# Kernel tuning notes

Hardware: AMD Instinct MI355X
Metric: run time of the kernel (lower is better)

## Reference

```python
import jax, jax.numpy as jnp
import numpy as np

N, E, D, H, O = 100000, 1600000, 128, 128, 64


def setup_inputs() -> dict:
    key = jax.random.key(0)
    ks = jax.random.split(key, 9)
    x = jax.random.normal(ks[0], (N, D), dtype=jnp.float32)
    edge_index = jax.random.randint(ks[1], (2, E), 0, N, dtype=jnp.int64)
    edge_weight = jax.random.normal(ks[2], (E,), dtype=jnp.float32)
    s1 = 1.0 / np.sqrt(D)
    s2 = 1.0 / np.sqrt(H)
    W_rel1 = jax.random.normal(ks[3], (D, H), dtype=jnp.float32) * s1
    b_rel1 = jnp.zeros((H,), dtype=jnp.float32)
    W_root1 = jax.random.normal(ks[4], (D, H), dtype=jnp.float32) * s1
    W_rel2 = jax.random.normal(ks[5], (H, O), dtype=jnp.float32) * s2
    b_rel2 = jnp.zeros((O,), dtype=jnp.float32)
    W_root2 = jax.random.normal(ks[6], (H, O), dtype=jnp.float32) * s2
    return {"x": x, "edge_weight": edge_weight, "edge_index": edge_index,
            "W_rel1": W_rel1, "b_rel1": b_rel1, "W_root1": W_root1,
            "W_rel2": W_rel2, "b_rel2": b_rel2, "W_root2": W_root2}


def _graph_conv(h, src, dst, ew, W_rel, b_rel, W_root):
    # message: gather source features, scale by edge weight  [E, d]
    msg = h[src] * ew[:, None]
    # aggregate: sum messages into destination nodes  [N, d]
    aggr = jax.ops.segment_sum(msg, dst, num_segments=N)
    # GraphConv: lin_rel(aggr) + lin_root(h)
    return aggr @ W_rel + b_rel + h @ W_root


def reference(x, edge_weight, edge_index, W_rel1, b_rel1, W_root1, W_rel2, b_rel2, W_root2):
    src, dst = edge_index[0], edge_index[1]
    ew = jax.nn.sigmoid(edge_weight)  # edge_weighted=True path, applied once
    h = jax.nn.relu(_graph_conv(x, src, dst, ew, W_rel1, b_rel1, W_root1))
    out = _graph_conv(h, src, dst, ew, W_rel2, b_rel2, W_root2)
    return out
```

## Files before the change

### kernel.cpp

```cpp
#include <hip/hip_runtime.h>

#define NN 100000
#define EE 1600000
#define DD 128
#define HH 128
#define OO 64

#define NPART 8
#define CAP 32
#define MAX_OVF 16384
#define CSTRIDE 16

typedef unsigned short u16;
typedef __attribute__((ext_vector_type(8))) short bf16x8;
typedef __attribute__((ext_vector_type(4))) float f32x4;

__device__ __forceinline__ u16 f2b(float f) {
  union { float f; unsigned u; } v; v.f = f;
  unsigned r = v.u + 0x7fffu + ((v.u >> 16) & 1u);
  return (u16)(r >> 16);
}
__device__ __forceinline__ float b2f(unsigned h) {
  union { unsigned u; float f; } v; v.u = h << 16;
  return v.f;
}
__device__ __forceinline__ void fma8(float* acc, uint4 v, float w) {
  acc[0] = fmaf(b2f(v.x & 0xffffu), w, acc[0]);
  acc[1] = fmaf(b2f(v.x >> 16), w, acc[1]);
  acc[2] = fmaf(b2f(v.y & 0xffffu), w, acc[2]);
  acc[3] = fmaf(b2f(v.y >> 16), w, acc[3]);
  acc[4] = fmaf(b2f(v.z & 0xffffu), w, acc[4]);
  acc[5] = fmaf(b2f(v.z >> 16), w, acc[5]);
  acc[6] = fmaf(b2f(v.w & 0xffffu), w, acc[6]);
  acc[7] = fmaf(b2f(v.w >> 16), w, acc[7]);
}

#define XB (NN * DD / 8 / 256)
__global__ __launch_bounds__(256) void cvt_k(
    const float* __restrict__ x, u16* __restrict__ xb,
    const float* __restrict__ Wr1, const float* __restrict__ Wo1,
    const float* __restrict__ Wr2, const float* __restrict__ Wo2,
    u16* __restrict__ Wt1, u16* __restrict__ Wt2) {
  if (blockIdx.x < XB) {
    int i = blockIdx.x * 256 + threadIdx.x;
    const float4* p = reinterpret_cast<const float4*>(x) + (size_t)i * 2;
    float4 a = p[0], b = p[1];
    uint4 o;
    o.x = (unsigned)f2b(a.x) | ((unsigned)f2b(a.y) << 16);
    o.y = (unsigned)f2b(a.z) | ((unsigned)f2b(a.w) << 16);
    o.z = (unsigned)f2b(b.x) | ((unsigned)f2b(b.y) << 16);
    o.w = (unsigned)f2b(b.z) | ((unsigned)f2b(b.w) << 16);
    reinterpret_cast<uint4*>(xb)[i] = o;
  } else {
    int i = (blockIdx.x - XB) * 256 + threadIdx.x;
    if (i < 128 * 256) {
      int n = i >> 8, k = i & 255;
      float v = (k < 128) ? Wr1[k * 128 + n] : Wo1[(k - 128) * 128 + n];
      Wt1[i] = f2b(v);
    } else if (i < 128 * 256 + 64 * 256) {
      int j = i - 128 * 256;
      int n = j >> 8, k = j & 255;
      float v = (k < 128) ? Wr2[k * 64 + n] : Wo2[(k - 128) * 64 + n];
      Wt2[j] = f2b(v);
    }
  }
}

__global__ __launch_bounds__(256) void fill_direct_k(
    const int* __restrict__ ei, const float* __restrict__ w,
    int* __restrict__ cntp, uint2* __restrict__ slots,
    uint4* __restrict__ ovf, int* __restrict__ ovf_cnt,
    int pstep, int E) {
  int part = blockIdx.x & (NPART - 1);
  int e = (blockIdx.x >> 3) * 256 + threadIdx.x;
  if (e >= E) return;
  int dst = ei[E + e];
  int lo = part * pstep;
  int hi = min(NN, lo + pstep);
  if (dst < lo || dst >= hi) return;
  int pos = atomicAdd(&cntp[dst * CSTRIDE], 1);
  float sig = 1.0f / (1.0f + expf(-w[e]));
  unsigned src = (unsigned)ei[e];
  if (pos < CAP) {
    slots[(size_t)dst * CAP + pos] = make_uint2(src, __float_as_uint(sig));
  } else {
    int o = atomicAdd(ovf_cnt, 1);
    if (o < MAX_OVF) ovf[o] = make_uint4((unsigned)dst, src, __float_as_uint(sig), 0u);
  }
}

__global__ __launch_bounds__(256) void gather_k(
    const u16* __restrict__ feat, const int* __restrict__ cntp,
    const uint2* __restrict__ slots, u16* __restrict__ aggr) {
  int gid = blockIdx.x * 256 + threadIdx.x;
  int node = gid >> 4;
  int c = gid & 15;
  if (node >= NN) return;
  int count = min(cntp[node * CSTRIDE], CAP);
  const uint2* recs = slots + (size_t)node * CAP;
  float acc[8] = {0.f, 0.f, 0.f, 0.f, 0.f, 0.f, 0.f, 0.f};
  int e = 0;
  for (; e + 8 <= count; e += 8) {
    uint2 r[8];
#pragma unroll
    for (int j = 0; j < 8; ++j) r[j] = recs[e + j];
    uint4 v[8];
#pragma unroll
    for (int j = 0; j < 8; ++j)
      v[j] = *reinterpret_cast<const uint4*>(feat + (size_t)r[j].x * DD + c * 8);
#pragma unroll
    for (int j = 0; j < 8; ++j) fma8(acc, v[j], __uint_as_float(r[j].y));
  }
  if (e + 4 <= count) {
    uint2 r[4];
#pragma unroll
    for (int j = 0; j < 4; ++j) r[j] = recs[e + j];
    uint4 v[4];
#pragma unroll
    for (int j = 0; j < 4; ++j)
      v[j] = *reinterpret_cast<const uint4*>(feat + (size_t)r[j].x * DD + c * 8);
#pragma unroll
    for (int j = 0; j < 4; ++j) fma8(acc, v[j], __uint_as_float(r[j].y));
    e += 4;
  }
  for (; e < count; ++e) {
    uint2 r = recs[e];
    uint4 v = *reinterpret_cast<const uint4*>(feat + (size_t)r.x * DD + c * 8);
    fma8(acc, v, __uint_as_float(r.y));
  }
  uint4 o;
  o.x = (unsigned)f2b(acc[0]) | ((unsigned)f2b(acc[1]) << 16);
  o.y = (unsigned)f2b(acc[2]) | ((unsigned)f2b(acc[3]) << 16);
  o.z = (unsigned)f2b(acc[4]) | ((unsigned)f2b(acc[5]) << 16);
  o.w = (unsigned)f2b(acc[6]) | ((unsigned)f2b(acc[7]) << 16);
  *reinterpret_cast<uint4*>(aggr + (size_t)node * DD + c * 8) = o;
}

__global__ __launch_bounds__(256) void ovf_fix_k(const int* __restrict__ ovf_cnt,
                                                 const uint4* __restrict__ ovf,
                                                 const u16* __restrict__ feat,
                                                 u16* __restrict__ aggr) {
  int novf = min(*ovf_cnt, MAX_OVF);
  int gid = blockIdx.x * 256 + threadIdx.x;
  int idx = gid >> 6;
  int word = gid & 63;
  if (idx >= novf) return;
  uint4 r = ovf[idx];
  float wgt = __uint_as_float(r.z);
  unsigned fv = *reinterpret_cast<const unsigned*>(feat + (size_t)r.y * DD + word * 2);
  float m0 = b2f(fv & 0xffffu) * wgt;
  float m1 = b2f(fv >> 16) * wgt;
  unsigned* addr = reinterpret_cast<unsigned*>(aggr + (size_t)r.x * DD + word * 2);
  unsigned old = *addr, assumed;
  do {
    assumed = old;
    float a0 = b2f(assumed & 0xffffu) + m0;
    float a1 = b2f(assumed >> 16) + m1;
    unsigned nv = (unsigned)f2b(a0) | ((unsigned)f2b(a1) << 16);
    old = atomicCAS(addr, assumed, nv);
  } while (old != assumed);
}

template <int HO, bool RELU, bool OUTBF16>
__global__ __launch_bounds__(256) void gemm_mfma_k(
    const u16* __restrict__ A1, const u16* __restrict__ A2,
    const u16* __restrict__ Bt, const float* __restrict__ bias,
    void* __restrict__ Cout, int n_rows) {
  constexpr int CG = HO / 16;
  __shared__ u16 As[64][40];
  __shared__ u16 Bs[HO][40];

  const int t = threadIdx.x;
  const int w = t >> 6;
  const int lane = t & 63;
  const int row0 = blockIdx.x * 64;

  f32x4 acc[CG];
#pragma unroll
  for (int cg = 0; cg < CG; ++cg) acc[cg] = (f32x4){0.f, 0.f, 0.f, 0.f};

  const int arow = w * 16 + (lane & 15);
  const int kq = (lane >> 4) * 8;

  for (int k0 = 0; k0 < 256; k0 += 32) {
    {
      int node = t >> 2;
      int koff = (t & 3) * 8;
      int k = k0 + koff;
      int gr = row0 + node;
      uint4 v = make_uint4(0u, 0u, 0u, 0u);
      if (gr < n_rows) {
        const u16* src = (k < 128) ? (A1 + (size_t)gr * 128 + k)
                                   : (A2 + (size_t)gr * 128 + (k - 128));
        v = *reinterpret_cast<const uint4*>(src);
      }
      *reinterpret_cast<uint4*>(&As[node][koff]) = v;
    }
#pragma unroll
    for (int i = 0; i < CG / 4; ++i) {
      int c2 = t + i * 256;
      int n = c2 >> 2;
      int koff = (c2 & 3) * 8;
      uint4 v = *reinterpret_cast<const uint4*>(Bt + (size_t)n * 256 + k0 + koff);
      *reinterpret_cast<uint4*>(&Bs[n][koff]) = v;
    }
    __syncthreads();

    bf16x8 a = *reinterpret_cast<const bf16x8*>(&As[arow][kq]);
#pragma unroll
    for (int cg = 0; cg < CG; ++cg) {
      bf16x8 b = *reinterpret_cast<const bf16x8*>(&Bs[cg * 16 + (lane & 15)][kq]);
      acc[cg] = __builtin_amdgcn_mfma_f32_16x16x32_bf16(a, b, acc[cg], 0, 0, 0);
    }
    __syncthreads();
  }

  const int rbase = w * 16 + ((lane >> 4) << 2);
#pragma unroll
  for (int cg = 0; cg < CG; ++cg) {
    int col = cg * 16 + (lane & 15);
    float bia = bias[col];
#pragma unroll
    for (int j = 0; j < 4; ++j) {
      int gr = row0 + rbase + j;
      if (gr < n_rows) {
        float v = acc[cg][j] + bia;
        if (RELU) v = fmaxf(v, 0.f);
        if (OUTBF16) ((u16*)Cout)[(size_t)gr * HO + col] = f2b(v);
        else ((float*)Cout)[(size_t)gr * HO + col] = v;
      }
    }
  }
}

extern "C" void kernel_launch(void* const* d_in, const int* in_sizes, int n_in,
                              void* d_out, int out_size, void* d_ws, size_t ws_size,
                              hipStream_t stream) {
  const float* x   = (const float*)d_in[0];
  const float* w   = (const float*)d_in[1];
  const int*   ei  = (const int*)d_in[2];
  const float* Wr1 = (const float*)d_in[3];
  const float* br1 = (const float*)d_in[4];
  const float* Wo1 = (const float*)d_in[5];
  const float* Wr2 = (const float*)d_in[6];
  const float* br2 = (const float*)d_in[7];
  const float* Wo2 = (const float*)d_in[8];
  float* out = (float*)d_out;

  char* ws = (char*)d_ws;
  int*   cntp    = (int*)(ws);
  int*   ovf_cnt = (int*)(ws + 6400000);
  uint4* ovf     = (uint4*)(ws + 6803072);
  uint2* slots   = (uint2*)(ws + 7065216);
  u16*   xb      = (u16*)(ws + 32665216);
  u16*   hb      = (u16*)(ws + 58265216);
  u16*   aggrb   = (u16*)(ws + 83865216);
  u16*   Wt1     = (u16*)(ws + 109465216);
  u16*   Wt2     = (u16*)(ws + 109530752);

  const int egrid = (EE + 255) / 256;

  cvt_k<<<XB + 192, 256, 0, stream>>>(x, xb, Wr1, Wo1, Wr2, Wo2, Wt1, Wt2);

  hipMemsetAsync(cntp, 0, 6401024, stream);
  {
    const int pstep = (NN + NPART - 1) / NPART;
    fill_direct_k<<<NPART * egrid, 256, 0, stream>>>(
        ei, w, cntp, slots, ovf, ovf_cnt, pstep, EE);
  }

  const int ggrid = (NN * 16 + 255) / 256;
  const int mgrid = (NN + 63) / 64;
  const int ogrid = (MAX_OVF * 64) / 256;

  gather_k<<<ggrid, 256, 0, stream>>>(xb, cntp, slots, aggrb);
  ovf_fix_k<<<ogrid, 256, 0, stream>>>(ovf_cnt, ovf, xb, aggrb);
  gemm_mfma_k<HH, true, true><<<mgrid, 256, 0, stream>>>(aggrb, xb, Wt1, br1, hb, NN);

  gather_k<<<ggrid, 256, 0, stream>>>(hb, cntp, slots, aggrb);
  ovf_fix_k<<<ogrid, 256, 0, stream>>>(ovf_cnt, ovf, hb, aggrb);
  gemm_mfma_k<OO, false, false><<<mgrid, 256, 0, stream>>>(aggrb, hb, Wt2, br2, out, NN);
}
```

Measured before the change: 255.5 us.

## Merge bucket fill and bf16 conversion into one kernel, drop dst partitioning

Merges the edge bucket-fill kernel with the x/weight bf16 conversion kernel into a single launch, with block ranges selecting the role. It also removes the 8-way destination partitioning, so each edge is read once instead of eight times. This cuts one launch and repeated edge-index reads, but the atomic scatter into slots loses the locality the partitioning gave it.

```diff
diff --git a/kernel.cpp b/kernel.cpp
--- a/kernel.cpp
+++ b/kernel.cpp
@@ -6,10 +6,13 @@
 #define HH 128
 #define OO 64
 
-#define NPART 8
 #define CAP 32
 #define MAX_OVF 16384
 #define CSTRIDE 16
+
+#define EGRID ((EE + 255) / 256)
+#define XBLK (NN * DD / 8 / 256)
+#define WBLK 192
 
 typedef unsigned short u16;
 typedef __attribute__((ext_vector_type(8))) short bf16x8;
@@ -35,24 +38,40 @@
   acc[7] = fmaf(b2f(v.w >> 16), w, acc[7]);
 }
 
-#define XB (NN * DD / 8 / 256)
-__global__ __launch_bounds__(256) void cvt_k(
+__global__ __launch_bounds__(256) void prep_fill_k(
+    const int* __restrict__ ei, const float* __restrict__ w,
+    int* __restrict__ cntp, uint2* __restrict__ slots,
+    uint4* __restrict__ ovf, int* __restrict__ ovf_cnt,
     const float* __restrict__ x, u16* __restrict__ xb,
     const float* __restrict__ Wr1, const float* __restrict__ Wo1,
     const float* __restrict__ Wr2, const float* __restrict__ Wo2,
     u16* __restrict__ Wt1, u16* __restrict__ Wt2) {
-  if (blockIdx.x < XB) {
-    int i = blockIdx.x * 256 + threadIdx.x;
+  const int b = blockIdx.x;
+  if (b < EGRID) {
+    int e = b * 256 + threadIdx.x;
+    if (e >= EE) return;
+    int dst = ei[EE + e];
+    int pos = atomicAdd(&cntp[dst * CSTRIDE], 1);
+    float sig = 1.0f / (1.0f + expf(-w[e]));
+    unsigned src = (unsigned)ei[e];
+    if (pos < CAP) {
+      slots[(size_t)dst * CAP + pos] = make_uint2(src, __float_as_uint(sig));
+    } else {
+      int o = atomicAdd(ovf_cnt, 1);
+      if (o < MAX_OVF) ovf[o] = make_uint4((unsigned)dst, src, __float_as_uint(sig), 0u);
+    }
+  } else if (b < EGRID + XBLK) {
+    int i = (b - EGRID) * 256 + threadIdx.x;
     const float4* p = reinterpret_cast<const float4*>(x) + (size_t)i * 2;
-    float4 a = p[0], b = p[1];
+    float4 a = p[0], bb = p[1];
     uint4 o;
     o.x = (unsigned)f2b(a.x) | ((unsigned)f2b(a.y) << 16);
     o.y = (unsigned)f2b(a.z) | ((unsigned)f2b(a.w) << 16);
-    o.z = (unsigned)f2b(b.x) | ((unsigned)f2b(b.y) << 16);
-    o.w = (unsigned)f2b(b.z) | ((unsigned)f2b(b.w) << 16);
+    o.z = (unsigned)f2b(bb.x) | ((unsigned)f2b(bb.y) << 16);
+    o.w = (unsigned)f2b(bb.z) | ((unsigned)f2b(bb.w) << 16);
     reinterpret_cast<uint4*>(xb)[i] = o;
   } else {
-    int i = (blockIdx.x - XB) * 256 + threadIdx.x;
+    int i = (b - EGRID - XBLK) * 256 + threadIdx.x;
     if (i < 128 * 256) {
       int n = i >> 8, k = i & 255;
       float v = (k < 128) ? Wr1[k * 128 + n] : Wo1[(k - 128) * 128 + n];
@@ -63,29 +82,6 @@
       float v = (k < 128) ? Wr2[k * 64 + n] : Wo2[(k - 128) * 64 + n];
       Wt2[j] = f2b(v);
     }
-  }
-}
-
-__global__ __launch_bounds__(256) void fill_direct_k(
-    const int* __restrict__ ei, const float* __restrict__ w,
-    int* __restrict__ cntp, uint2* __restrict__ slots,
-    uint4* __restrict__ ovf, int* __restrict__ ovf_cnt,
-    int pstep, int E) {
-  int part = blockIdx.x & (NPART - 1);
-  int e = (blockIdx.x >> 3) * 256 + threadIdx.x;
-  if (e >= E) return;
-  int dst = ei[E + e];
-  int lo = part * pstep;
-  int hi = min(NN, lo + pstep);
-  if (dst < lo || dst >= hi) return;
-  int pos = atomicAdd(&cntp[dst * CSTRIDE], 1);
-  float sig = 1.0f / (1.0f + expf(-w[e]));
-  unsigned src = (unsigned)ei[e];
-  if (pos < CAP) {
-    slots[(size_t)dst * CAP + pos] = make_uint2(src, __float_as_uint(sig));
-  } else {
-    int o = atomicAdd(ovf_cnt, 1);
-    if (o < MAX_OVF) ovf[o] = make_uint4((unsigned)dst, src, __float_as_uint(sig), 0u);
   }
 }
 
@@ -258,16 +254,10 @@
   u16*   Wt1     = (u16*)(ws + 109465216);
   u16*   Wt2     = (u16*)(ws + 109530752);
 
-  const int egrid = (EE + 255) / 256;
-
-  cvt_k<<<XB + 192, 256, 0, stream>>>(x, xb, Wr1, Wo1, Wr2, Wo2, Wt1, Wt2);
-
   hipMemsetAsync(cntp, 0, 6401024, stream);
-  {
-    const int pstep = (NN + NPART - 1) / NPART;
-    fill_direct_k<<<NPART * egrid, 256, 0, stream>>>(
-        ei, w, cntp, slots, ovf, ovf_cnt, pstep, EE);
-  }
+  prep_fill_k<<<EGRID + XBLK + WBLK, 256, 0, stream>>>(
+      ei, w, cntp, slots, ovf, ovf_cnt,
+      x, xb, Wr1, Wo1, Wr2, Wo2, Wt1, Wt2);
 
   const int ggrid = (NN * 16 + 255) / 256;
   const int mgrid = (NN + 63) / 64;
```

Result: slower. 329.2 us (+28.8%).
